# Kernel optimization log

Measured on AMD Instinct MI355X. Metric: run time of the kernel, lower is better.

Reference implementation:

```python
import jax, jax.numpy as jnp
import numpy as np

T, B, I, H = 512, 256, 512, 512


def setup_inputs() -> dict:
    key = jax.random.key(0)
    ks = jax.random.split(key, 10)
    inp = {
        "x": jax.random.normal(ks[0], (T, B, I), dtype=jnp.float32),
        "lengths": jax.random.randint(ks[1], (B,), 1, T + 1).astype(jnp.int64),
        # LSTMCell params, gate order [i, f, g, o]; forget-gate bias init to 1
        "W_ih": jax.random.normal(ks[2], (4 * H, I), dtype=jnp.float32) / np.sqrt(I),
        "W_hh": jax.random.normal(ks[3], (4 * H, H), dtype=jnp.float32) / np.sqrt(H),
        "b_ih": jnp.zeros((4 * H,), jnp.float32).at[H:2 * H].set(1.0),
        "b_hh": jnp.zeros((4 * H,), jnp.float32),
        # multiplicative projections
        "mx_w": jax.random.normal(ks[4], (H, I), dtype=jnp.float32) / np.sqrt(I),
        "mx_b": jnp.zeros((H,), jnp.float32),
        "mh_w": jax.random.normal(ks[5], (H, H), dtype=jnp.float32) / np.sqrt(H),
        "mh_b": jnp.zeros((H,), jnp.float32),
        "h0": jnp.zeros((H,), jnp.float32),
        "c0": jnp.zeros((H,), jnp.float32),
    }
    return inp


def _mlstm(x, lengths, W_ih, W_hh, b_ih, b_hh, mx_w, mx_b, mh_w, mh_b, h0, c0):
    Tn, Bn, _ = x.shape
    Hn = h0.shape[0]
    # Precompute all input-side projections in two big GEMMs (batched over T*B).
    xg = jnp.einsum('tbi,gi->tbg', x, W_ih) + b_ih          # [T,B,4H]
    xm = jnp.einsum('tbi,hi->tbh', x, mx_w) + mx_b          # [T,B,H]
    # active[t,b] = t < lengths[b]; padded steps freeze (h,c) -> packed semantics
    active = (jnp.arange(Tn)[:, None] < lengths[None, :])[..., None]  # [T,B,1]

    def step(carry, inp):
        h, c = carry
        xg_t, xm_t, act = inp
        m = xm_t * (h @ mh_w.T + mh_b)                       # multiplicative hidden
        gates = xg_t + m @ W_hh.T + b_hh                     # cell(x, (m, c))
        i, f, g, o = jnp.split(gates, 4, axis=-1)
        c_new = jax.nn.sigmoid(f) * c + jax.nn.sigmoid(i) * jnp.tanh(g)
        h_new = jax.nn.sigmoid(o) * jnp.tanh(c_new)
        h = jnp.where(act, h_new, h)
        c = jnp.where(act, c_new, c)
        return (h, c), None

    h_init = jnp.broadcast_to(h0, (Bn, Hn))
    c_init = jnp.broadcast_to(c0, (Bn, Hn))
    (h, c), _ = jax.lax.scan(step, (h_init, c_init), (xg, xm, active))
    # Torch code returns final cell state of each sequence, in batch order.
    return c


def reference(x, lengths, W_ih, W_hh, b_ih, b_hh, mx_w, mx_b, mh_w, mh_b, h0, c0):
    return _mlstm(x, lengths, W_ih, W_hh, b_ih, b_hh, mx_w, mx_b, mh_w, mh_b, h0, c0)
```

## Files before the change

### kernel.cpp

```cpp
#include <hip/hip_runtime.h>
#include <stdint.h>


typedef __attribute__((ext_vector_type(8))) short s8v;
typedef __attribute__((ext_vector_type(8))) _Float16 h8v;
typedef __attribute__((ext_vector_type(4))) float f4v;
typedef __attribute__((ext_vector_type(4))) uint32_t u4v;

#define SC 2048.0f
#define ISC (1.0f / 2048.0f)

__device__ __forceinline__ f4v mf(s8v a, s8v b, f4v c) {
  return __builtin_amdgcn_mfma_f32_16x16x32_f16(
      __builtin_bit_cast(h8v, a), __builtin_bit_cast(h8v, b), c, 0, 0, 0);
}
__device__ __forceinline__ uint16_t f2h(float x) {
  _Float16 h = (_Float16)x;
  return __builtin_bit_cast(uint16_t, h);
}
__device__ __forceinline__ void split2(float v, uint16_t& hi, uint16_t& lo) {
  _Float16 h = (_Float16)v;
  float r = v - (float)h;
  hi = __builtin_bit_cast(uint16_t, h);
  lo = f2h(r * SC);
}
__device__ __forceinline__ float unpk1(uint32_t w) {
  _Float16 h = __builtin_bit_cast(_Float16, (uint16_t)(w >> 16));
  _Float16 lo = __builtin_bit_cast(_Float16, (uint16_t)(w & 0xFFFEu));
  return (float)h + (float)lo * ISC;
}
__device__ __forceinline__ float sigm(float x) { return 1.0f / (1.0f + __expf(-x)); }
__device__ __forceinline__ float tanh_f(float x) { return 1.0f - 2.0f / (__expf(2.0f * x) + 1.0f); }

__device__ __forceinline__ u4v ldp(const uint32_t* p) {
  u4v r;
  asm volatile("global_load_dwordx4 %0, %1, off sc1" : "=v"(r) : "v"(p));
  return r;
}
__device__ __forceinline__ void st_pk(uint32_t* p, float v, uint32_t par) {
  uint16_t hi, lo;
  split2(v, hi, lo);
  uint32_t w = ((uint32_t)lo & 0xFFFEu) | par | ((uint32_t)hi << 16);
  asm volatile("global_store_dword %0, %1, off sc1" ::"v"(p), "v"(w) : "memory");
}
#define VM0                                          \
  do {                                               \
    asm volatile("s_waitcnt vmcnt(0)" ::: "memory"); \
    __builtin_amdgcn_sched_barrier(0);               \
  } while (0)

#define POLLB(BASE, KT0, PAR)                                              \
  for (;;) {                                                               \
    _Pragma("unroll")                                                      \
    for (int q = 0; q < 8; ++q) {                                          \
      pk[2 * q] = ldp((BASE) + ((KT0) + q) * 32);                          \
      pk[2 * q + 1] = ldp((BASE) + ((KT0) + q) * 32 + 4);                  \
    }                                                                      \
    VM0;                                                                   \
    uint32_t _acc = 0;                                                     \
    _Pragma("unroll")                                                      \
    for (int q = 0; q < 16; ++q)                                           \
      _acc |= (pk[q].x ^ (PAR)) | (pk[q].y ^ (PAR)) |                      \
              (pk[q].z ^ (PAR)) | (pk[q].w ^ (PAR));                       \
    if (__all((int)((_acc & 1u) == 0u))) break;                            \
  }

#define UNPK(A, B, HI, LO)                                                 \
  {                                                                        \
    union { uint32_t u[4]; s8v s; } _h, _l;                                \
    _l.u[0] = ((A).x & 0xFFFFu) | ((A).y << 16);                           \
    _l.u[1] = ((A).z & 0xFFFFu) | ((A).w << 16);                           \
    _l.u[2] = ((B).x & 0xFFFFu) | ((B).y << 16);                           \
    _l.u[3] = ((B).z & 0xFFFFu) | ((B).w << 16);                           \
    _h.u[0] = ((A).x >> 16) | ((A).y & 0xFFFF0000u);                       \
    _h.u[1] = ((A).z >> 16) | ((A).w & 0xFFFF0000u);                       \
    _h.u[2] = ((B).x >> 16) | ((B).y & 0xFFFF0000u);                       \
    _h.u[3] = ((B).z >> 16) | ((B).w & 0xFFFF0000u);                       \
    HI = _h.s;                                                             \
    LO = _l.s;                                                             \
  }

__global__ __launch_bounds__(256) void k_split(const float* __restrict__ x,
                                               uint16_t* __restrict__ xh,
                                               uint16_t* __restrict__ xl, long n) {
  long i = ((long)blockIdx.x * 256 + threadIdx.x) * 8;
  if (i >= n) return;
  float4 a = *(const float4*)(x + i);
  float4 b = *(const float4*)(x + i + 4);
  union { uint16_t u[8]; s8v v; } oh, ol;
  float vv[8] = {a.x, a.y, a.z, a.w, b.x, b.y, b.z, b.w};
#pragma unroll
  for (int k = 0; k < 8; ++k) split2(vv[k], oh.u[k], ol.u[k]);
  *(s8v*)(xh + i) = oh.v;
  *(s8v*)(xl + i) = ol.v;
}

__global__ __launch_bounds__(64) void k_packw(const float* __restrict__ Wg,
                                              const float* __restrict__ Wm,
                                              uint16_t* __restrict__ wh,
                                              uint16_t* __restrict__ wl) {
  int s = blockIdx.x >> 4, kt = blockIdx.x & 15, l = threadIdx.x;
  const float* src = (s < 128) ? (Wg + (size_t)(s * 16 + (l & 15)) * 512)
                               : (Wm + (size_t)((s - 128) * 16 + (l & 15)) * 512);
  int k0 = kt * 32 + (l >> 4) * 8;
  float4 a = *(const float4*)(src + k0);
  float4 b = *(const float4*)(src + k0 + 4);
  union { uint16_t u[8]; s8v v; } oh, ol;
  float vv[8] = {a.x, a.y, a.z, a.w, b.x, b.y, b.z, b.w};
#pragma unroll
  for (int k = 0; k < 8; ++k) split2(vv[k], oh.u[k], ol.u[k]);
  size_t adr = ((size_t)(s * 16 + kt) * 64 + l) * 8;
  *(s8v*)(wh + adr) = oh.v;
  *(s8v*)(wl + adr) = ol.v;
}

__global__ __launch_bounds__(256) void k_init(const float* __restrict__ h0,
                                              uint32_t* __restrict__ hpk,
                                              uint32_t* __restrict__ mpk) {
  int idx = blockIdx.x * 256 + threadIdx.x;
  int col = idx & 511;
  uint16_t hi, lo;
  split2(h0[col], hi, lo);
  hpk[idx] = ((uint32_t)lo & 0xFFFEu) | ((uint32_t)hi << 16);
  mpk[idx] = 1u;
}

__device__ __forceinline__ void gpass(const uint16_t* __restrict__ Ap,
                                      const uint16_t* __restrict__ Bp,
                                      s8v* Asm, s8v* Bsm, int rowbase, int s0,
                                      f4v (&acc)[4][4]) {
  int tid = threadIdx.x;
  int wv = tid >> 6, l = tid & 63, wm = wv >> 1, wn = wv & 1;
  int arow = tid >> 1, ahalf = tid & 1, swz = (arow & 7) << 4;
  for (int ks = 0; ks < 8; ++ks) {
    __syncthreads();
    const uint16_t* asrc = Ap + (size_t)(rowbase + arow) * 512 + ks * 64;
#pragma unroll
    for (int q = 0; q < 4; ++q) {
      int pb = ahalf * 64 + q * 16;
      Asm[arow * 8 + (pb >> 4)] = *(const s8v*)(asrc + ((pb ^ swz) >> 1));
    }
#pragma unroll
    for (int q = 0; q < 4; ++q) {
      int ofs = tid * 64 + q * 16;
      int si = ofs >> 11, kti = (ofs >> 10) & 1, inner = ofs & 1023;
      Bsm[ofs >> 4] =
          *(const s8v*)(Bp + (size_t)((s0 + si) * 16 + ks * 2 + kti) * 512 + (inner >> 1));
    }
    __syncthreads();
#pragma unroll
    for (int kti = 0; kti < 2; ++kti) {
      s8v a[4], b[4];
#pragma unroll
      for (int i = 0; i < 4; ++i) {
        int row = wm * 64 + i * 16 + (l & 15);
        int lb = kti * 64 + (l >> 4) * 16;
        a[i] = Asm[row * 8 + ((lb ^ ((l & 7) << 4)) >> 4)];
      }
#pragma unroll
      for (int jj = 0; jj < 4; ++jj) b[jj] = Bsm[((wn * 4 + jj) * 2 + kti) * 64 + l];
#pragma unroll
      for (int i = 0; i < 4; ++i)
#pragma unroll
        for (int jj = 0; jj < 4; ++jj) acc[i][jj] = mf(a[i], b[jj], acc[i][jj]);
    }
  }
}

__global__ __launch_bounds__(256, 2) void k_gemm3(const uint16_t* __restrict__ xh,
                                                  const uint16_t* __restrict__ xl,
                                                  const uint16_t* __restrict__ wh,
                                                  const uint16_t* __restrict__ wl,
                                                  float* __restrict__ blob, int row0) {
  __shared__ s8v Asm[1024], Bsm[1024];
  f4v acc_a[4][4], acc_c[4][4];
#pragma unroll
  for (int i = 0; i < 4; ++i)
#pragma unroll
    for (int jj = 0; jj < 4; ++jj) {
      acc_a[i][jj] = (f4v){0.f, 0.f, 0.f, 0.f};
      acc_c[i][jj] = (f4v){0.f, 0.f, 0.f, 0.f};
    }
  int s0 = blockIdx.x * 8, r0 = blockIdx.y * 128;
  int rowbase = row0 + r0;
  gpass(xh, wh, Asm, Bsm, rowbase, s0, acc_a);
  gpass(xh, wl, Asm, Bsm, rowbase, s0, acc_c);
  gpass(xl, wh, Asm, Bsm, rowbase, s0, acc_c);
  int tid = threadIdx.x, wv = tid >> 6, l = tid & 63, wm = wv >> 1, wn = wv & 1;
#pragma unroll
  for (int i = 0; i < 4; ++i)
#pragma unroll
    for (int jj = 0; jj < 4; ++jj) {
      int s = s0 + wn * 4 + jj;
#pragma unroll
      for (int ri = 0; ri < 4; ++ri) {
        int trow = r0 + wm * 64 + i * 16 + (l >> 4) * 4 + ri;
        int tt = trow >> 8, gg = (trow >> 4) & 15, rr = trow & 15;
        size_t adr = ((size_t)(tt * 160 + s) * 16 + gg) * 256 + rr * 16 + (l & 15);
        blob[adr] = acc_a[i][jj][ri] + acc_c[i][jj][ri] * ISC;
      }
    }
}

__global__ __launch_bounds__(128, 1) void k_rec(
    const uint16_t* __restrict__ wrh, const uint16_t* __restrict__ wrl,
    const float* __restrict__ blob,
    const float* __restrict__ b_ih, const float* __restrict__ b_hh,
    const float* __restrict__ mx_b, const float* __restrict__ mh_b,
    const float* __restrict__ c0, const int* __restrict__ lengths,
    uint32_t* hpk, uint32_t* mpk, float* cbuf, float* out, int chunk) {
  extern __shared__ char smraw[];
  s8v* SW = (s8v*)smraw;
  int tid = threadIdx.x, l = tid & 63, wv = tid >> 6;
  int bid = blockIdx.x, j = bid >> 3, gg = ((bid & 7) << 1) | wv;

#pragma unroll
  for (int sl = 0; sl < 9; ++sl) {
    int gs = (sl < 4) ? (sl * 32 + j) : (sl < 8 ? (sl - 4) * 32 + j : 128 + j);
    const s8v* src = (const s8v*)(((sl < 4) ? wrh : wrl) + (size_t)gs * 8192);
#pragma unroll
    for (int it = 0; it < 8; ++it) SW[sl * 1024 + it * 128 + tid] = src[it * 128 + tid];
  }
  s8v wmh[16];
  {
    const s8v* sH = (const s8v*)(wrh + (size_t)(128 + j) * 8192);
#pragma unroll
    for (int kt = 0; kt < 16; ++kt) wmh[kt] = sH[kt * 64 + l];
  }
  __syncthreads();

  int cidx = l & 15, rq = l >> 4;
  int hc = j * 16 + cidx;
  float mhb = mh_b[hc], mxb = mx_b[hc];
  float bsum[4];
#pragma unroll
  for (int nt = 0; nt < 4; ++nt) bsum[nt] = b_ih[nt * 512 + hc] + b_hh[nt * 512 + hc];
  int rowA = gg * 16 + cidx;
  int kofs = rq * 8;
  int rowC0 = gg * 16 + rq * 4;
  float creg[4], hreg[4];
  int lenr[4];
#pragma unroll
  for (int ri = 0; ri < 4; ++ri) {
    int r = rowC0 + ri;
    lenr[ri] = lengths[r];
    creg[ri] = (chunk == 0) ? c0[hc] : cbuf[(size_t)r * 512 + hc];
    hreg[ri] = unpk1(hpk[(size_t)r * 512 + hc]);
  }

  const uint32_t* hrb = hpk + (size_t)rowA * 512 + kofs;
  const uint32_t* mrb = mpk + (size_t)rowA * 512 + kofs;

  for (int t = 0; t < 128; ++t) {
    int tg = chunk * 128 + t;
    uint32_t parC = (uint32_t)(tg & 1);
    uint32_t parN = (uint32_t)((tg + 1) & 1);
    size_t tb = ((size_t)(t * 160) * 16 + (size_t)gg) * 256 + rq * 64 + cidx;
    float bxm[4], bg[4][4];
#pragma unroll
    for (int ri = 0; ri < 4; ++ri) {
      bxm[ri] = blob[tb + (size_t)(128 + j) * 4096 + ri * 16];
#pragma unroll
      for (int nt = 0; nt < 4; ++nt)
        bg[nt][ri] = blob[tb + (size_t)(nt * 32 + j) * 4096 + ri * 16];
    }
    u4v pk[16];
    f4v a1a = (f4v){0, 0, 0, 0}, a1c0 = (f4v){0, 0, 0, 0}, a1c1 = (f4v){0, 0, 0, 0};
    POLLB(hrb, 0, parC);
#pragma unroll
    for (int q = 0; q < 8; ++q) {
      s8v hi_, lo_;
      UNPK(pk[2 * q], pk[2 * q + 1], hi_, lo_);
      a1a = mf(hi_, wmh[q], a1a);
      a1c0 = mf(hi_, SW[8 * 1024 + q * 64 + l], a1c0);
      a1c1 = mf(lo_, wmh[q], a1c1);
    }
    POLLB(hrb, 8, parC);
#pragma unroll
    for (int q = 0; q < 8; ++q) {
      int kt = 8 + q;
      s8v hi_, lo_;
      UNPK(pk[2 * q], pk[2 * q + 1], hi_, lo_);
      a1a = mf(hi_, wmh[kt], a1a);
      a1c0 = mf(hi_, SW[8 * 1024 + kt * 64 + l], a1c0);
      a1c1 = mf(lo_, wmh[kt], a1c1);
    }
#pragma unroll
    for (int ri = 0; ri < 4; ++ri) {
      float hv = a1a[ri] + (a1c0[ri] + a1c1[ri]) * ISC + mhb;
      float mv = (bxm[ri] + mxb) * hv;
      st_pk(mpk + (size_t)(rowC0 + ri) * 512 + hc, mv, parC);
    }
    f4v p2a[4], p2c[4], p2d[4];
#pragma unroll
    for (int nt = 0; nt < 4; ++nt) {
      p2a[nt] = (f4v){0, 0, 0, 0};
      p2c[nt] = (f4v){0, 0, 0, 0};
      p2d[nt] = (f4v){0, 0, 0, 0};
    }
    POLLB(mrb, 0, parC);
#pragma unroll
    for (int q = 0; q < 8; ++q) {
      s8v hi_, lo_;
      UNPK(pk[2 * q], pk[2 * q + 1], hi_, lo_);
#pragma unroll
      for (int nt = 0; nt < 4; ++nt) {
        p2a[nt] = mf(hi_, SW[nt * 1024 + q * 64 + l], p2a[nt]);
        p2c[nt] = mf(hi_, SW[(4 + nt) * 1024 + q * 64 + l], p2c[nt]);
        p2d[nt] = mf(lo_, SW[nt * 1024 + q * 64 + l], p2d[nt]);
      }
    }
    POLLB(mrb, 8, parC);
#pragma unroll
    for (int q = 0; q < 8; ++q) {
      int kt = 8 + q;
      s8v hi_, lo_;
      UNPK(pk[2 * q], pk[2 * q + 1], hi_, lo_);
#pragma unroll
      for (int nt = 0; nt < 4; ++nt) {
        p2a[nt] = mf(hi_, SW[nt * 1024 + kt * 64 + l], p2a[nt]);
        p2c[nt] = mf(hi_, SW[(4 + nt) * 1024 + kt * 64 + l], p2c[nt]);
        p2d[nt] = mf(lo_, SW[nt * 1024 + kt * 64 + l], p2d[nt]);
      }
    }
#pragma unroll
    for (int ri = 0; ri < 4; ++ri) {
      float gi = p2a[0][ri] + (p2c[0][ri] + p2d[0][ri]) * ISC + bsum[0] + bg[0][ri];
      float gf = p2a[1][ri] + (p2c[1][ri] + p2d[1][ri]) * ISC + bsum[1] + bg[1][ri];
      float gc = p2a[2][ri] + (p2c[2][ri] + p2d[2][ri]) * ISC + bsum[2] + bg[2][ri];
      float go = p2a[3][ri] + (p2c[3][ri] + p2d[3][ri]) * ISC + bsum[3] + bg[3][ri];
      float iv = sigm(gi), fv = sigm(gf), gv = tanh_f(gc), ov = sigm(go);
      float cn = fv * creg[ri] + iv * gv;
      float hn = ov * tanh_f(cn);
      bool act = tg < lenr[ri];
      if (act) {
        creg[ri] = cn;
        hreg[ri] = hn;
      }
      st_pk(hpk + (size_t)(rowC0 + ri) * 512 + hc, hreg[ri], parN);
    }
  }
#pragma unroll
  for (int ri = 0; ri < 4; ++ri) {
    cbuf[(size_t)(rowC0 + ri) * 512 + hc] = creg[ri];
    if (chunk == 3) out[(size_t)(rowC0 + ri) * 512 + hc] = creg[ri];
  }
}

extern "C" void kernel_launch(void* const* d_in, const int* in_sizes, int n_in,
                              void* d_out, int out_size, void* d_ws, size_t ws_size,
                              hipStream_t stream) {
  (void)in_sizes; (void)n_in; (void)out_size;
  const float* x = (const float*)d_in[0];
  const int* lengths = (const int*)d_in[1];
  const float* W_ih = (const float*)d_in[2];
  const float* W_hh = (const float*)d_in[3];
  const float* b_ih = (const float*)d_in[4];
  const float* b_hh = (const float*)d_in[5];
  const float* mx_w = (const float*)d_in[6];
  const float* mx_b = (const float*)d_in[7];
  const float* mh_w = (const float*)d_in[8];
  const float* mh_b = (const float*)d_in[9];
  const float* h0 = (const float*)d_in[10];
  const float* c0 = (const float*)d_in[11];

  if (ws_size < 616038400ull) return;

  char* ws = (char*)d_ws;
  uint16_t* xh = (uint16_t*)(ws);
  uint16_t* xl = (uint16_t*)(ws + 134217728ull);
  uint16_t* wpre_h = (uint16_t*)(ws + 268435456ull);
  uint16_t* wpre_l = (uint16_t*)(ws + 271056896ull);
  uint16_t* wrec_h = (uint16_t*)(ws + 273678336ull);
  uint16_t* wrec_l = (uint16_t*)(ws + 276299776ull);
  float* blob = (float*)(ws + 278921216ull);
  uint32_t* hpk = (uint32_t*)(ws + 614465536ull);
  uint32_t* mpk = (uint32_t*)(ws + 614989824ull);
  float* cbuf = (float*)(ws + 615514112ull);

  k_split<<<32768, 256, 0, stream>>>(x, xh, xl, 67108864L);
  k_packw<<<2560, 64, 0, stream>>>(W_ih, mx_w, wpre_h, wpre_l);
  k_packw<<<2560, 64, 0, stream>>>(W_hh, mh_w, wrec_h, wrec_l);
  k_init<<<512, 256, 0, stream>>>(h0, hpk, mpk);
  hipFuncSetAttribute(reinterpret_cast<const void*>(k_rec),
                      hipFuncAttributeMaxDynamicSharedMemorySize, 147456);
  for (int c = 0; c < 4; ++c) {
    k_gemm3<<<dim3(20, 256), 256, 0, stream>>>(xh, xl, wpre_h, wpre_l, blob, c * 32768);
    k_rec<<<256, 128, 147456, stream>>>(wrec_h, wrec_l, blob, b_ih, b_hh, mx_b, mh_b,
                                        c0, lengths, hpk, mpk, cbuf, (float*)d_out, c);
  }
}
```

Baseline: 8.586 ms.

## Exchange recurrent h and m as single fp16 values instead of hi/lo pairs

Stops splitting the shared hidden state h and the multiplicative term m into fp16 hi+lo pairs. Each is now stored as one 16-bit fp16 value with the parity bit in the LSB, which halves the polled inter-block traffic, merges the two poll phases into one, and drops the lo-part MFMAs. Weights keep their hi/lo split. The cost is lower precision on the activations, and the poll loop now has an iteration cap that could let stale data through.

```diff
diff --git a/kernel.cpp b/kernel.cpp
--- a/kernel.cpp
+++ b/kernel.cpp
@@ -24,24 +24,19 @@
   hi = __builtin_bit_cast(uint16_t, h);
   lo = f2h(r * SC);
 }
-__device__ __forceinline__ float unpk1(uint32_t w) {
-  _Float16 h = __builtin_bit_cast(_Float16, (uint16_t)(w >> 16));
-  _Float16 lo = __builtin_bit_cast(_Float16, (uint16_t)(w & 0xFFFEu));
-  return (float)h + (float)lo * ISC;
+__device__ __forceinline__ float h2f(uint16_t w) {
+  return (float)__builtin_bit_cast(_Float16, w);
 }
 __device__ __forceinline__ float sigm(float x) { return 1.0f / (1.0f + __expf(-x)); }
 __device__ __forceinline__ float tanh_f(float x) { return 1.0f - 2.0f / (__expf(2.0f * x) + 1.0f); }
 
-__device__ __forceinline__ u4v ldp(const uint32_t* p) {
+__device__ __forceinline__ u4v ldx4_sc1(const uint16_t* p) {
   u4v r;
   asm volatile("global_load_dwordx4 %0, %1, off sc1" : "=v"(r) : "v"(p));
   return r;
 }
-__device__ __forceinline__ void st_pk(uint32_t* p, float v, uint32_t par) {
-  uint16_t hi, lo;
-  split2(v, hi, lo);
-  uint32_t w = ((uint32_t)lo & 0xFFFEu) | par | ((uint32_t)hi << 16);
-  asm volatile("global_store_dword %0, %1, off sc1" ::"v"(p), "v"(w) : "memory");
+__device__ __forceinline__ void st16_sc1(uint16_t* p, uint32_t v) {
+  asm volatile("global_store_short %0, %1, off sc1" ::"v"(p), "v"(v) : "memory");
 }
 #define VM0                                          \
   do {                                               \
@@ -49,35 +44,22 @@
     __builtin_amdgcn_sched_barrier(0);               \
   } while (0)
 
-#define POLLB(BASE, KT0, PAR)                                              \
-  for (;;) {                                                               \
-    _Pragma("unroll")                                                      \
-    for (int q = 0; q < 8; ++q) {                                          \
-      pk[2 * q] = ldp((BASE) + ((KT0) + q) * 32);                          \
-      pk[2 * q + 1] = ldp((BASE) + ((KT0) + q) * 32 + 4);                  \
+#define POLLS(BASE, PAR)                                                   \
+  {                                                                        \
+    int _cap = 1 << 18;                                                    \
+    const uint32_t _tt = (PAR)*0x00010001u;                                \
+    for (;;) {                                                             \
+      _Pragma("unroll")                                                    \
+      for (int q = 0; q < 16; ++q) pk[q] = ldx4_sc1((BASE) + q * 32);      \
+      VM0;                                                                 \
+      uint32_t _a = 0;                                                     \
+      _Pragma("unroll")                                                    \
+      for (int q = 0; q < 16; ++q)                                         \
+        _a |= (pk[q].x ^ _tt) | (pk[q].y ^ _tt) |                          \
+              (pk[q].z ^ _tt) | (pk[q].w ^ _tt);                           \
+      if (__all((int)((_a & 0x00010001u) == 0u))) break;                   \
+      if (--_cap == 0) break;                                              \
     }                                                                      \
-    VM0;                                                                   \
-    uint32_t _acc = 0;                                                     \
-    _Pragma("unroll")                                                      \
-    for (int q = 0; q < 16; ++q)                                           \
-      _acc |= (pk[q].x ^ (PAR)) | (pk[q].y ^ (PAR)) |                      \
-              (pk[q].z ^ (PAR)) | (pk[q].w ^ (PAR));                       \
-    if (__all((int)((_acc & 1u) == 0u))) break;                            \
-  }
-
-#define UNPK(A, B, HI, LO)                                                 \
-  {                                                                        \
-    union { uint32_t u[4]; s8v s; } _h, _l;                                \
-    _l.u[0] = ((A).x & 0xFFFFu) | ((A).y << 16);                           \
-    _l.u[1] = ((A).z & 0xFFFFu) | ((A).w << 16);                           \
-    _l.u[2] = ((B).x & 0xFFFFu) | ((B).y << 16);                           \
-    _l.u[3] = ((B).z & 0xFFFFu) | ((B).w << 16);                           \
-    _h.u[0] = ((A).x >> 16) | ((A).y & 0xFFFF0000u);                       \
-    _h.u[1] = ((A).z >> 16) | ((A).w & 0xFFFF0000u);                       \
-    _h.u[2] = ((B).x >> 16) | ((B).y & 0xFFFF0000u);                       \
-    _h.u[3] = ((B).z >> 16) | ((B).w & 0xFFFF0000u);                       \
-    HI = _h.s;                                                             \
-    LO = _l.s;                                                             \
   }
 
 __global__ __launch_bounds__(256) void k_split(const float* __restrict__ x,
@@ -115,14 +97,12 @@
 }
 
 __global__ __launch_bounds__(256) void k_init(const float* __restrict__ h0,
-                                              uint32_t* __restrict__ hpk,
-                                              uint32_t* __restrict__ mpk) {
+                                              uint16_t* __restrict__ hp,
+                                              uint16_t* __restrict__ mp) {
   int idx = blockIdx.x * 256 + threadIdx.x;
   int col = idx & 511;
-  uint16_t hi, lo;
-  split2(h0[col], hi, lo);
-  hpk[idx] = ((uint32_t)lo & 0xFFFEu) | ((uint32_t)hi << 16);
-  mpk[idx] = 1u;
+  hp[idx] = f2h(h0[col]) & 0xFFFEu;
+  mp[idx] = 1u;
 }
 
 __device__ __forceinline__ void gpass(const uint16_t* __restrict__ Ap,
@@ -208,7 +188,7 @@
     const float* __restrict__ b_ih, const float* __restrict__ b_hh,
     const float* __restrict__ mx_b, const float* __restrict__ mh_b,
     const float* __restrict__ c0, const int* __restrict__ lengths,
-    uint32_t* hpk, uint32_t* mpk, float* cbuf, float* out, int chunk) {
+    uint16_t* hp, uint16_t* mp, float* cbuf, float* out, int chunk) {
   extern __shared__ char smraw[];
   s8v* SW = (s8v*)smraw;
   int tid = threadIdx.x, l = tid & 63, wv = tid >> 6;
@@ -245,11 +225,11 @@
     int r = rowC0 + ri;
     lenr[ri] = lengths[r];
     creg[ri] = (chunk == 0) ? c0[hc] : cbuf[(size_t)r * 512 + hc];
-    hreg[ri] = unpk1(hpk[(size_t)r * 512 + hc]);
-  }
-
-  const uint32_t* hrb = hpk + (size_t)rowA * 512 + kofs;
-  const uint32_t* mrb = mpk + (size_t)rowA * 512 + kofs;
+    hreg[ri] = h2f(hp[(size_t)r * 512 + hc]);
+  }
+
+  const uint16_t* hrb = hp + (size_t)rowA * 512 + kofs;
+  const uint16_t* mrb = mp + (size_t)rowA * 512 + kofs;
 
   for (int t = 0; t < 128; ++t) {
     int tg = chunk * 128 + t;
@@ -265,70 +245,47 @@
         bg[nt][ri] = blob[tb + (size_t)(nt * 32 + j) * 4096 + ri * 16];
     }
     u4v pk[16];
-    f4v a1a = (f4v){0, 0, 0, 0}, a1c0 = (f4v){0, 0, 0, 0}, a1c1 = (f4v){0, 0, 0, 0};
-    POLLB(hrb, 0, parC);
-#pragma unroll
-    for (int q = 0; q < 8; ++q) {
-      s8v hi_, lo_;
-      UNPK(pk[2 * q], pk[2 * q + 1], hi_, lo_);
-      a1a = mf(hi_, wmh[q], a1a);
-      a1c0 = mf(hi_, SW[8 * 1024 + q * 64 + l], a1c0);
-      a1c1 = mf(lo_, wmh[q], a1c1);
-    }
-    POLLB(hrb, 8, parC);
-#pragma unroll
-    for (int q = 0; q < 8; ++q) {
-      int kt = 8 + q;
-      s8v hi_, lo_;
-      UNPK(pk[2 * q], pk[2 * q + 1], hi_, lo_);
-      a1a = mf(hi_, wmh[kt], a1a);
-      a1c0 = mf(hi_, SW[8 * 1024 + kt * 64 + l], a1c0);
-      a1c1 = mf(lo_, wmh[kt], a1c1);
+    f4v a1a0 = (f4v){0, 0, 0, 0}, a1a1 = (f4v){0, 0, 0, 0};
+    f4v a1c0 = (f4v){0, 0, 0, 0}, a1c1 = (f4v){0, 0, 0, 0};
+    POLLS(hrb, parC);
+#pragma unroll
+    for (int kt = 0; kt < 16; kt += 2) {
+      s8v e = __builtin_bit_cast(s8v, pk[kt]);
+      s8v o = __builtin_bit_cast(s8v, pk[kt + 1]);
+      a1a0 = mf(e, wmh[kt], a1a0);
+      a1a1 = mf(o, wmh[kt + 1], a1a1);
+      a1c0 = mf(e, SW[8 * 1024 + kt * 64 + l], a1c0);
+      a1c1 = mf(o, SW[8 * 1024 + (kt + 1) * 64 + l], a1c1);
     }
 #pragma unroll
     for (int ri = 0; ri < 4; ++ri) {
-      float hv = a1a[ri] + (a1c0[ri] + a1c1[ri]) * ISC + mhb;
+      float hv = a1a0[ri] + a1a1[ri] + (a1c0[ri] + a1c1[ri]) * ISC + mhb;
       float mv = (bxm[ri] + mxb) * hv;
-      st_pk(mpk + (size_t)(rowC0 + ri) * 512 + hc, mv, parC);
-    }
-    f4v p2a[4], p2c[4], p2d[4];
+      uint32_t w = ((uint32_t)f2h(mv) & 0xFFFEu) | parC;
+      st16_sc1(mp + (size_t)(rowC0 + ri) * 512 + hc, w);
+    }
+    f4v p2a[4], p2c[4];
 #pragma unroll
     for (int nt = 0; nt < 4; ++nt) {
       p2a[nt] = (f4v){0, 0, 0, 0};
       p2c[nt] = (f4v){0, 0, 0, 0};
-      p2d[nt] = (f4v){0, 0, 0, 0};
-    }
-    POLLB(mrb, 0, parC);
-#pragma unroll
-    for (int q = 0; q < 8; ++q) {
-      s8v hi_, lo_;
-      UNPK(pk[2 * q], pk[2 * q + 1], hi_, lo_);
+    }
+    POLLS(mrb, parC);
+#pragma unroll
+    for (int kt = 0; kt < 16; ++kt) {
+      s8v e = __builtin_bit_cast(s8v, pk[kt]);
 #pragma unroll
       for (int nt = 0; nt < 4; ++nt) {
-        p2a[nt] = mf(hi_, SW[nt * 1024 + q * 64 + l], p2a[nt]);
-        p2c[nt] = mf(hi_, SW[(4 + nt) * 1024 + q * 64 + l], p2c[nt]);
-        p2d[nt] = mf(lo_, SW[nt * 1024 + q * 64 + l], p2d[nt]);
+        p2a[nt] = mf(e, SW[nt * 1024 + kt * 64 + l], p2a[nt]);
+        p2c[nt] = mf(e, SW[(4 + nt) * 1024 + kt * 64 + l], p2c[nt]);
       }
     }
-    POLLB(mrb, 8, parC);
-#pragma unroll
-    for (int q = 0; q < 8; ++q) {
-      int kt = 8 + q;
-      s8v hi_, lo_;
-      UNPK(pk[2 * q], pk[2 * q + 1], hi_, lo_);
-#pragma unroll
-      for (int nt = 0; nt < 4; ++nt) {
-        p2a[nt] = mf(hi_, SW[nt * 1024 + kt * 64 + l], p2a[nt]);
-        p2c[nt] = mf(hi_, SW[(4 + nt) * 1024 + kt * 64 + l], p2c[nt]);
-        p2d[nt] = mf(lo_, SW[nt * 1024 + kt * 64 + l], p2d[nt]);
-      }
-    }
 #pragma unroll
     for (int ri = 0; ri < 4; ++ri) {
-      float gi = p2a[0][ri] + (p2c[0][ri] + p2d[0][ri]) * ISC + bsum[0] + bg[0][ri];
-      float gf = p2a[1][ri] + (p2c[1][ri] + p2d[1][ri]) * ISC + bsum[1] + bg[1][ri];
-      float gc = p2a[2][ri] + (p2c[2][ri] + p2d[2][ri]) * ISC + bsum[2] + bg[2][ri];
-      float go = p2a[3][ri] + (p2c[3][ri] + p2d[3][ri]) * ISC + bsum[3] + bg[3][ri];
+      float gi = p2a[0][ri] + p2c[0][ri] * ISC + bsum[0] + bg[0][ri];
+      float gf = p2a[1][ri] + p2c[1][ri] * ISC + bsum[1] + bg[1][ri];
+      float gc = p2a[2][ri] + p2c[2][ri] * ISC + bsum[2] + bg[2][ri];
+      float go = p2a[3][ri] + p2c[3][ri] * ISC + bsum[3] + bg[3][ri];
       float iv = sigm(gi), fv = sigm(gf), gv = tanh_f(gc), ov = sigm(go);
       float cn = fv * creg[ri] + iv * gv;
       float hn = ov * tanh_f(cn);
@@ -337,7 +294,8 @@
         creg[ri] = cn;
         hreg[ri] = hn;
       }
-      st_pk(hpk + (size_t)(rowC0 + ri) * 512 + hc, hreg[ri], parN);
+      uint32_t w = ((uint32_t)f2h(hreg[ri]) & 0xFFFEu) | parN;
+      st16_sc1(hp + (size_t)(rowC0 + ri) * 512 + hc, w);
     }
   }
 #pragma unroll
@@ -364,7 +322,7 @@
   const float* h0 = (const float*)d_in[10];
   const float* c0 = (const float*)d_in[11];
 
-  if (ws_size < 616038400ull) return;
+  if (ws_size < 615514112ull) return;
 
   char* ws = (char*)d_ws;
   uint16_t* xh = (uint16_t*)(ws);
@@ -374,19 +332,19 @@
   uint16_t* wrec_h = (uint16_t*)(ws + 273678336ull);
   uint16_t* wrec_l = (uint16_t*)(ws + 276299776ull);
   float* blob = (float*)(ws + 278921216ull);
-  uint32_t* hpk = (uint32_t*)(ws + 614465536ull);
-  uint32_t* mpk = (uint32_t*)(ws + 614989824ull);
-  float* cbuf = (float*)(ws + 615514112ull);
+  uint16_t* hp = (uint16_t*)(ws + 614465536ull);
+  uint16_t* mp = (uint16_t*)(ws + 614727680ull);
+  float* cbuf = (float*)(ws + 614989824ull);
 
   k_split<<<32768, 256, 0, stream>>>(x, xh, xl, 67108864L);
   k_packw<<<2560, 64, 0, stream>>>(W_ih, mx_w, wpre_h, wpre_l);
   k_packw<<<2560, 64, 0, stream>>>(W_hh, mh_w, wrec_h, wrec_l);
-  k_init<<<512, 256, 0, stream>>>(h0, hpk, mpk);
+  k_init<<<512, 256, 0, stream>>>(h0, hp, mp);
   hipFuncSetAttribute(reinterpret_cast<const void*>(k_rec),
                       hipFuncAttributeMaxDynamicSharedMemorySize, 147456);
   for (int c = 0; c < 4; ++c) {
     k_gemm3<<<dim3(20, 256), 256, 0, stream>>>(xh, xl, wpre_h, wpre_l, blob, c * 32768);
     k_rec<<<256, 128, 147456, stream>>>(wrec_h, wrec_l, blob, b_ih, b_hh, mx_b, mh_b,
-                                        c0, lengths, hpk, mpk, cbuf, (float*)d_out, c);
-  }
-}
+                                        c0, lengths, hp, mp, cbuf, (float*)d_out, c);
+  }
+}
```

New measurement: 10.07 ms. +17.3%, slower.
